# Performance work log

Measured on AMD Instinct MI355X. Metric: run time of the kernel, lower is better.

Reference implementation:

```python
import jax, jax.numpy as jnp
import numpy as np

L, T, R = 2, 2, 2          # layers, node types (0=user,1=movie), edge types
NU, NM, E = 50000, 10000, 500000
C, H, DPHI = 128, 4, 64
D = C // H                 # head dim = 32
SQRT_D = float(np.sqrt(D))


def setup_inputs() -> dict:
    key = jax.random.key(0)
    ks = jax.random.split(key, 16)
    s = 0.05
    src = jax.random.randint(ks[0], (E,), 0, NU)
    dst = jax.random.randint(ks[1], (E,), 0, NM)
    return {
        "user_emb": jax.random.normal(ks[2], (NU, C)) * 0.01,
        "movie_emb": jax.random.normal(ks[3], (NM, C)) * 0.01,
        "phi": jax.random.normal(ks[4], (NM, DPHI)),
        "meta_w": jax.random.normal(ks[5], (DPHI, C)) * s,
        "meta_b": jnp.zeros((C,)),
        "kw": jax.random.normal(ks[6], (L, T, C, C)) * s,
        "kb": jnp.zeros((L, T, C)),
        "qw": jax.random.normal(ks[7], (L, T, C, C)) * s,
        "qb": jnp.zeros((L, T, C)),
        "vw": jax.random.normal(ks[8], (L, T, C, C)) * s,
        "vb": jnp.zeros((L, T, C)),
        "a_rel": jax.random.normal(ks[9], (L, R, H, D, D)) * s,
        "m_rel": jax.random.normal(ks[10], (L, R, H, D, D)) * s,
        "p_rel": jnp.ones((L, R, H)),
        "ow": jax.random.normal(ks[11], (L, T, C, C)) * s,
        "ob": jnp.zeros((L, T, C)),
        "skip": jnp.ones((L, T)),
        "edge_index": jnp.stack([src, dst]),  # [2,E], row0=user idx, row1=movie idx
    }


def _segment_softmax(logits, seg, n):
    # logits: [E,H], seg: [E] destination node ids
    m = jax.ops.segment_max(logits, seg, num_segments=n)
    e = jnp.exp(logits - m[seg])
    s = jax.ops.segment_sum(e, seg, num_segments=n)
    return e / (s[seg] + 1e-16)


def _hgt_layer(xs, kw, kb, qw, qb, vw, vb, a_rel, m_rel, p_rel, ow, ob, skip, edge_index):
    ns = [x.shape[0] for x in xs]
    k = [(xs[t] @ kw[t] + kb[t]).reshape(ns[t], H, D) for t in range(T)]
    q = [(xs[t] @ qw[t] + qb[t]).reshape(ns[t], H, D) for t in range(T)]
    v = [(xs[t] @ vw[t] + vb[t]).reshape(ns[t], H, D) for t in range(T)]
    # edge types: r=0 user->movie, r=1 movie->user (reverse)
    etypes = [(0, 1, edge_index[0], edge_index[1]),
              (1, 0, edge_index[1], edge_index[0])]
    agg = [jnp.zeros((ns[t], C), dtype=xs[t].dtype) for t in range(T)]
    for r, (st, dt, src, dst) in enumerate(etypes):
        ke = jnp.einsum('nhd,hde->nhe', k[st], a_rel[r])   # per-edge-type key transform
        ve = jnp.einsum('nhd,hde->nhe', v[st], m_rel[r])
        logits = (q[dt][dst] * ke[src]).sum(-1) * p_rel[r] / SQRT_D   # [E,H]
        alpha = _segment_softmax(logits, dst, ns[dt])                  # [E,H]
        msg = (alpha[:, :, None] * ve[src]).reshape(-1, C)
        agg[dt] = agg[dt] + jax.ops.segment_sum(msg, dst, num_segments=ns[dt])
    out = []
    for t in range(T):
        o = jax.nn.gelu(agg[t]) @ ow[t] + ob[t]
        g = jax.nn.sigmoid(skip[t])
        out.append(g * o + (1.0 - g) * xs[t])
    return out


def reference(user_emb, movie_emb, phi, meta_w, meta_b, kw, kb, qw, qb, vw, vb,
              a_rel, m_rel, p_rel, ow, ob, skip, edge_index):
    xu = user_emb
    xm = movie_emb + phi @ meta_w + meta_b   # meta feature fusion on movie nodes
    xs = [xu, xm]
    for l in range(L):
        xs = _hgt_layer(xs, kw[l], kb[l], qw[l], qb[l], vw[l], vb[l],
                        a_rel[l], m_rel[l], p_rel[l], ow[l], ob[l], skip[l], edge_index)
    return (xs[0], xs[1])
```

## Files before the change

kernel.cpp:

```cpp
#include <hip/hip_runtime.h>
#include <hip/hip_bf16.h>

#define Cc 128
#define Hh 4
#define Dd 32
#define DPHI2 64
#define Ll 2
#define Tt 2
#define Rr 2

typedef __hip_bfloat16 bf16;
using short8 = __attribute__((ext_vector_type(8))) short;
using f32x4 = __attribute__((ext_vector_type(4))) float;
using f32x2 = __attribute__((ext_vector_type(2))) float;
typedef _Float16 h2 __attribute__((ext_vector_type(2)));
typedef __fp16 fp16x2 __attribute__((ext_vector_type(2)));

__device__ __forceinline__ unsigned short f2bf(float f) {
  union { float f; unsigned u; } v; v.f = f;
  unsigned r = v.u + 0x7fff + ((v.u >> 16) & 1);
  return (unsigned short)(r >> 16);
}
__device__ __forceinline__ h2 u2h(unsigned u) {
  union { unsigned u; h2 h; } v; v.u = u; return v.h;
}
__device__ __forceinline__ unsigned pkh(float a, float b) {
  union { unsigned u; fp16x2 h; } v;
  v.h = __builtin_amdgcn_cvt_pkrtz(a, b);
  return v.u;
}

__device__ __forceinline__ float fp8_decode1(unsigned char b) {
  unsigned u = b & 0x7f;
  float nrm = __builtin_bit_cast(float, (u << 20) + 0x3C000000u);
  float sub = (float)u * 0.001953125f;
  float v = (u >= 8) ? nrm : sub;
  return (b & 0x80) ? -v : v;
}
template <bool HI>
__device__ __forceinline__ f32x2 fp8x2f(unsigned w) {
#if __has_builtin(__builtin_amdgcn_cvt_pk_f32_fp8)
  return __builtin_amdgcn_cvt_pk_f32_fp8(w, HI);
#else
  unsigned b = HI ? (w >> 16) : (w & 0xffff);
  f32x2 r;
  r[0] = fp8_decode1((unsigned char)b);
  r[1] = fp8_decode1((unsigned char)(b >> 8));
  return r;
#endif
}
#if !__has_builtin(__builtin_amdgcn_cvt_pk_fp8_f32)
__device__ __forceinline__ unsigned char fp8_encode1(float f) {
  unsigned s = (__builtin_bit_cast(unsigned, f) >> 31) << 7;
  float a = fabsf(f);
  a = fminf(a, 448.f);
  unsigned char out;
  if (a < 0.0009765625f) {
    out = 0;
  } else if (a < 0.015625f) {
    out = (unsigned char)(a * 512.f + 0.5f);
  } else {
    unsigned bits = __builtin_bit_cast(unsigned, a);
    int e = (int)(bits >> 23) - 127;
    unsigned m = (bits >> 20) & 7;
    m += (bits >> 19) & 1;
    unsigned ee = (unsigned)(e + 7);
    if (m == 8) { m = 0; ee += 1; }
    if (ee > 15) { ee = 15; m = 6; }
    out = (unsigned char)((ee << 3) | m);
  }
  return out | (unsigned char)s;
}
#endif
__device__ __forceinline__ unsigned pk_fp8x4(float v0, float v1, float v2, float v3) {
#if __has_builtin(__builtin_amdgcn_cvt_pk_fp8_f32)
  int p = __builtin_amdgcn_cvt_pk_fp8_f32(v0, v1, 0, false);
  p = __builtin_amdgcn_cvt_pk_fp8_f32(v2, v3, p, true);
  return (unsigned)p;
#else
  return (unsigned)fp8_encode1(v0) | ((unsigned)fp8_encode1(v1) << 8) |
         ((unsigned)fp8_encode1(v2) << 16) | ((unsigned)fp8_encode1(v3) << 24);
#endif
}

__device__ __forceinline__ float dpp_add_xor1(float x) {
  int v = __builtin_amdgcn_update_dpp(0, __builtin_bit_cast(int, x), 0xB1, 0xF, 0xF, true);
  return x + __builtin_bit_cast(float, v);
}
__device__ __forceinline__ float dpp_add_xor2(float x) {
  int v = __builtin_amdgcn_update_dpp(0, __builtin_bit_cast(int, x), 0x4E, 0xF, 0xF, true);
  return x + __builtin_bit_cast(float, v);
}

__device__ __forceinline__ float gelu_tanh(float x) {
  float u = 0.7978845608028654f * (x + 0.044715f * x * x * x);
  float t = 1.f - 2.f / (__expf(2.f * u) + 1.f);
  return 0.5f * x * (1.f + t);
}

__device__ __forceinline__ void gload_lds16(const void* gsrc, void* lds) {
  __builtin_amdgcn_global_load_lds(
      (const __attribute__((address_space(1))) unsigned int*)gsrc,
      (__attribute__((address_space(3))) unsigned int*)lds, 16, 0, 0);
}

__global__ __launch_bounds__(256) void setup_kernel(
    const int* __restrict__ esrc, const int* __restrict__ edst, int E_, int NM_, int NU_,
    int* __restrict__ cnt, int* __restrict__ eoffm, int* __restrict__ eoffu,
    const float* __restrict__ kw, const float* __restrict__ kb,
    const float* __restrict__ qw, const float* __restrict__ qb,
    const float* __restrict__ vw, const float* __restrict__ vb,
    const float* __restrict__ a_rel, const float* __restrict__ m_rel,
    const float* __restrict__ p_rel, const float* __restrict__ ow,
    const float* __restrict__ ob,
    unsigned short* __restrict__ WT, float* __restrict__ bQKV,
    unsigned short* __restrict__ OWT, float* __restrict__ bO,
    const float* __restrict__ ue, const float* __restrict__ me,
    const float* __restrict__ phi, const float* __restrict__ mw,
    const float* __restrict__ mb,
    float* __restrict__ xout, unsigned short* __restrict__ Xb,
    int HB, int PB) {
  int b = blockIdx.x;
  if (b < HB) {
    int base_e = b * 2048;
#pragma unroll
    for (int j = 0; j < 8; ++j) {
      int e = base_e + j * 256 + (int)threadIdx.x;
      if (e < E_) {
        eoffm[e] = atomicAdd(&cnt[edst[e]], 1);
        eoffu[e] = atomicAdd(&cnt[NM_ + esrc[e]], 1);
      }
    }
    return;
  }
  if (b < HB + PB) {
    int idx = (b - HB) * 2 + (threadIdx.x >> 7);
    int g = idx >> 2, lt = idx & 3;
    int l = lt >> 1, t = lt & 1, r = t;
    int k = threadIdx.x & 127;
    const float inv_sqrt_d = 0.17677669529663687f;
    const float QSCALE = 1.4426950408889634f / 256.f;
    float val, bval;
    if (g < 128) {
      val = qw[((size_t)lt * Cc + k) * Cc + g] * QSCALE;
      bval = qb[(size_t)lt * Cc + g] * QSCALE;
    } else if (g < 384) {
      int isV = (g >= 256);
      int n = g - (isV ? 256 : 128);
      int h = n >> 5, e = n & 31;
      const float* W = (isV ? vw : kw) + (size_t)lt * Cc * Cc;
      const float* bb = (isV ? vb : kb) + (size_t)lt * Cc;
      const float* Ah = (isV ? m_rel : a_rel) + (((size_t)l * Rr + r) * Hh + h) * Dd * Dd;
      float s = 0.f, sb = 0.f;
      for (int d = 0; d < Dd; ++d) {
        float ae = Ah[d * Dd + e];
        s += W[(size_t)k * Cc + h * Dd + d] * ae;
        sb += bb[h * Dd + d] * ae;
      }
      float scale = isV ? 256.f : p_rel[((size_t)l * Rr + r) * Hh + h] * inv_sqrt_d * 256.f;
      val = s * scale;
      bval = sb * scale;
    } else {
      int n = g - 384;
      val = ow[((size_t)lt * Cc + k) * Cc + n];
      bval = ob[(size_t)lt * Cc + n];
    }
    if (g < 384) {
      WT[((size_t)lt * 384 + g) * Cc + k] = f2bf(val);
      if (k == 0) bQKV[(size_t)lt * 384 + g] = bval;
    } else {
      OWT[((size_t)lt * Cc + (g - 384)) * Cc + k] = f2bf(val);
      if (k == 0) bO[(size_t)lt * Cc + (g - 384)] = bval;
    }
    return;
  }
  int i4 = (b - HB - PB) * 256 + threadIdx.x;
  int totalU4 = NU_ * 32;
  float4 s;
  size_t o;
  if (i4 < totalU4) {
    o = (size_t)i4 * 4;
    s = *(const float4*)&ue[o];
  } else {
    int mg = i4 - totalU4;
    if (mg >= NM_ * 32) return;
    int m = mg >> 5, c = (mg & 31) * 4;
    o = (size_t)(NU_ * 32 + mg) * 4;
    s = *(const float4*)&me[(size_t)m * Cc + c];
    float4 bmv = *(const float4*)&mb[c];
    s.x += bmv.x; s.y += bmv.y; s.z += bmv.z; s.w += bmv.w;
    const float* ph = phi + (size_t)m * DPHI2;
#pragma unroll 4
    for (int d = 0; d < DPHI2; ++d) {
      float p = ph[d];
      float4 w4 = *(const float4*)&mw[d * Cc + c];
      s.x += p * w4.x; s.y += p * w4.y; s.z += p * w4.z; s.w += p * w4.w;
    }
  }
  *(float4*)&xout[o] = s;
  uint2 pk;
  pk.x = (unsigned)f2bf(s.x) | ((unsigned)f2bf(s.y) << 16);
  pk.y = (unsigned)f2bf(s.z) | ((unsigned)f2bf(s.w) << 16);
  *(uint2*)&Xb[o] = pk;
}

__global__ __launch_bounds__(256) void scan_p1(const int* __restrict__ cnt, int n,
                                               int* __restrict__ psum) {
  int i0 = blockIdx.x * 1024 + threadIdx.x * 4;
  int s = 0;
#pragma unroll
  for (int j = 0; j < 4; ++j) {
    int i = i0 + j;
    if (i < n) s += cnt[i];
  }
#pragma unroll
  for (int off = 1; off < 64; off <<= 1) s += __shfl_xor(s, off, 64);
  __shared__ int wsum[4];
  if ((threadIdx.x & 63) == 0) wsum[threadIdx.x >> 6] = s;
  __syncthreads();
  if (threadIdx.x == 0) psum[blockIdx.x] = wsum[0] + wsum[1] + wsum[2] + wsum[3];
}
__global__ void scan_p2(int* psum, int nb) {
  if (threadIdx.x == 0 && blockIdx.x == 0) {
    int run = 0;
    for (int i = 0; i < nb; ++i) { int v = psum[i]; psum[i] = run; run += v; }
  }
}
__global__ __launch_bounds__(256) void scan_p3(const int* __restrict__ cnt, int n,
                                               const int* __restrict__ psum,
                                               int* __restrict__ rowptr) {
  __shared__ int sdata[256];
  int i0 = blockIdx.x * 1024 + threadIdx.x * 4;
  int a0 = (i0 + 0 < n) ? cnt[i0 + 0] : 0;
  int a1 = (i0 + 1 < n) ? cnt[i0 + 1] : 0;
  int a2 = (i0 + 2 < n) ? cnt[i0 + 2] : 0;
  int a3 = (i0 + 3 < n) ? cnt[i0 + 3] : 0;
  int s = a0 + a1 + a2 + a3;
  sdata[threadIdx.x] = s;
  __syncthreads();
  for (int off = 1; off < 256; off <<= 1) {
    int t = ((int)threadIdx.x >= off) ? sdata[threadIdx.x - off] : 0;
    __syncthreads();
    sdata[threadIdx.x] += t;
    __syncthreads();
  }
  int run = psum[blockIdx.x] + sdata[threadIdx.x] - s;
  if (i0 + 0 < n) rowptr[i0 + 1] = run + a0;
  if (i0 + 1 < n) rowptr[i0 + 2] = run + a0 + a1;
  if (i0 + 2 < n) rowptr[i0 + 3] = run + a0 + a1 + a2;
  if (i0 + 3 < n) rowptr[i0 + 4] = run + s;
  if (blockIdx.x == 0 && threadIdx.x == 0) rowptr[0] = 0;
}

template <int NCH, int MODE>
__global__ __launch_bounds__(256, 2) void mfma_gemm(
    int NBU_, int NU_, int NM_,
    const bf16* __restrict__ Abase,
    const bf16* __restrict__ WTl, const float* __restrict__ biasl,
    char* __restrict__ Qc, char* __restrict__ KVc,
    float* __restrict__ xout, unsigned short* __restrict__ Xb,
    const float* __restrict__ skipl,
    int GB, const int* __restrict__ esrc, const int* __restrict__ edst, int E_,
    const int* __restrict__ rowptr, const int* __restrict__ eoffm,
    const int* __restrict__ eoffu, int* __restrict__ srcAll) {
  __shared__ char Bs[2][16384];
  if ((int)blockIdx.x >= GB) {
    int e = ((int)blockIdx.x - GB) * 256 + threadIdx.x;
    if (e < E_) {
      int s = esrc[e], d = edst[e];
      srcAll[rowptr[d] + eoffm[e]] = s << 8;
      srcAll[rowptr[NM_ + s] + eoffu[e]] = (NU_ + d) << 8;
    }
    return;
  }
  int bx = blockIdx.x;
  int t, row0, M, base;
  if (bx < NBU_) { t = 0; row0 = bx * 128; M = NU_; base = 0; }
  else { t = 1; row0 = (bx - NBU_) * 128; M = NM_; base = NU_; }
  const char* BT = (const char*)(WTl + (size_t)t * (NCH * 64) * Cc);
  const float* bias = biasl + (size_t)t * (NCH * 64);
  int wid = threadIdx.x >> 6, lane = threadIdx.x & 63;
  int rw = row0 + wid * 32;
  bool wact = rw < M;
  int lr = lane & 15, lk8 = (lane >> 4) * 8;

  auto stage = [&](int ch, int buf) {
    const char* src = BT + (size_t)ch * 16384;
#pragma unroll
    for (int j = 0; j < 4; ++j) {
      int u = wid * 4 + j;
      int d = u * 1024 + lane * 16;
      int g = d ^ (((d >> 8) & 7) << 4);
      gload_lds16(src + g, &Bs[buf][u * 1024]);
    }
  };

  short8 a[2][4];
#pragma unroll
  for (int mt = 0; mt < 2; ++mt) {
    int r = rw + mt * 16 + lr;
    const bf16* ap = Abase + (size_t)(base + r) * Cc + lk8;
#pragma unroll
    for (int kk = 0; kk < 4; ++kk) {
      short8 v = {};
      if (wact && r < M) v = *(const short8*)(ap + kk * 32);
      a[mt][kk] = v;
    }
  }
  float g = 0.f;
  if (MODE == 1) g = 1.f / (1.f + __expf(-skipl[t]));

  stage(0, 0);
#pragma unroll
  for (int ch = 0; ch < NCH; ++ch) {
    int buf = ch & 1;
    __syncthreads();
    if (ch + 1 < NCH) stage(ch + 1, buf ^ 1);
    short8 b[4][4];
#pragma unroll
    for (int nt = 0; nt < 4; ++nt) {
      int r = nt * 16 + lr;
#pragma unroll
      for (int kk = 0; kk < 4; ++kk) {
        int a0 = r * 256 + (lk8 + kk * 32) * 2;
        b[nt][kk] = *(const short8*)(&Bs[buf][a0 ^ ((r & 7) << 4)]);
      }
    }
    f32x4 acc[2][4];
#pragma unroll
    for (int mt = 0; mt < 2; ++mt)
#pragma unroll
      for (int nt = 0; nt < 4; ++nt) acc[mt][nt] = (f32x4){0.f, 0.f, 0.f, 0.f};
#pragma unroll
    for (int kk = 0; kk < 4; ++kk)
#pragma unroll
      for (int mt = 0; mt < 2; ++mt)
#pragma unroll
        for (int nt = 0; nt < 4; ++nt)
          acc[mt][nt] = __builtin_amdgcn_mfma_f32_16x16x32_bf16(
              b[nt][kk], a[mt][kk], acc[mt][nt], 0, 0, 0);
    if (!wact) continue;
#pragma unroll
    for (int mt = 0; mt < 2; ++mt) {
      int r = rw + mt * 16 + lr;
      if (r >= M) continue;
      size_t grow = (size_t)(base + r);
#pragma unroll
      for (int nt = 0; nt < 4; ++nt) {
        int cb = ch * 64 + nt * 16 + 4 * (lane >> 4);
        float4 b4 = *(const float4*)&bias[cb];
        float v0 = acc[mt][nt][0] + b4.x;
        float v1 = acc[mt][nt][1] + b4.y;
        float v2 = acc[mt][nt][2] + b4.z;
        float v3 = acc[mt][nt][3] + b4.w;
        if (MODE == 0) {
          if (cb < Cc) {
            uint2 pk;
            pk.x = pkh(v0, v1); pk.y = pkh(v2, v3);
            *(uint2*)(Qc + grow * 256 + cb * 2) = pk;
          } else {
            int c = cb - 128;
            int isv = c >> 7; c &= 127;
            int off = (c >> 3) * 16 + (c & 7) + isv * 8;
            unsigned pk = pk_fp8x4(v0, v1, v2, v3);
            *(unsigned*)(KVc + grow * 256 + off) = pk;
          }
        } else {
          float* xp = xout + grow * Cc + cb;
          float4 old = *(const float4*)xp;
          float n0 = g * v0 + (1.f - g) * old.x;
          float n1 = g * v1 + (1.f - g) * old.y;
          float n2 = g * v2 + (1.f - g) * old.z;
          float n3 = g * v3 + (1.f - g) * old.w;
          *(float4*)xp = make_float4(n0, n1, n2, n3);
          uint2 pk;
          pk.x = (unsigned)f2bf(n0) | ((unsigned)f2bf(n1) << 16);
          pk.y = (unsigned)f2bf(n2) | ((unsigned)f2bf(n3) << 16);
          *(uint2*)(Xb + grow * Cc + cb) = pk;
        }
      }
    }
  }
}

__global__ __launch_bounds__(256) void agg_kernel(
    const int* __restrict__ rowptr, const int* __restrict__ srcAll,
    const char* __restrict__ Qc, const char* __restrict__ KVc,
    unsigned short* __restrict__ AGGb, int NM_, int NU_) {
  int wid = threadIdx.x >> 6, lane = threadIdx.x & 63;
  int sub = lane & 15, eo = lane >> 4;
  int NT_ = NM_ + NU_;
  int W = (blockIdx.x * 4 + wid) * 4 + eo;
  bool active = W < NT_;
  int Wc = active ? W : NT_ - 1;
  int beg = rowptr[Wc];
  int end = active ? rowptr[Wc + 1] : beg;
  int dnode = (Wc < NM_) ? (NU_ + Wc) : (Wc - NM_);
  int myoff = sub * 16;
  uint4 qv = *(const uint4*)(Qc + (size_t)dnode * 256 + myoff);
  float qf0, qf1, qf2, qf3, qf4, qf5, qf6, qf7;
  {
    h2 t0 = u2h(qv.x), t1 = u2h(qv.y), t2 = u2h(qv.z), t3 = u2h(qv.w);
    qf0 = (float)t0[0]; qf1 = (float)t0[1];
    qf2 = (float)t1[0]; qf3 = (float)t1[1];
    qf4 = (float)t2[0]; qf5 = (float)t2[1];
    qf6 = (float)t3[0]; qf7 = (float)t3[1];
  }
  float acc0 = 0.f, acc1 = 0.f, acc2 = 0.f, acc3 = 0.f;
  float acc4 = 0.f, acc5 = 0.f, acc6 = 0.f, acc7 = 0.f;
  float denom = 0.f;
  const char* KVp = KVc + myoff;

#define CONSUME(KV, WVALID)                                                       \
  {                                                                               \
    f32x2 k01 = fp8x2f<false>((KV).x), k23 = fp8x2f<true>((KV).x);                \
    f32x2 k45 = fp8x2f<false>((KV).y), k67 = fp8x2f<true>((KV).y);                \
    float pA = qf0 * k01[0] + qf1 * k01[1] + qf2 * k23[0] + qf3 * k23[1];         \
    float pB = qf4 * k45[0] + qf5 * k45[1] + qf6 * k67[0] + qf7 * k67[1];         \
    float p = pA + pB;                                                            \
    p = dpp_add_xor1(p);                                                          \
    p = dpp_add_xor2(p);                                                          \
    float w = (WVALID) ? exp2f(p) : 0.f;                                          \
    denom += w;                                                                   \
    f32x2 v01 = fp8x2f<false>((KV).z), v23 = fp8x2f<true>((KV).z);                \
    f32x2 v45 = fp8x2f<false>((KV).w), v67 = fp8x2f<true>((KV).w);                \
    acc0 += w * v01[0]; acc1 += w * v01[1];                                       \
    acc2 += w * v23[0]; acc3 += w * v23[1];                                       \
    acc4 += w * v45[0]; acc5 += w * v45[1];                                       \
    acc6 += w * v67[0]; acc7 += w * v67[1];                                       \
  }

  for (int e = beg; __any(e < end); e += 4) {
    bool v0 = e < end, v1 = (e + 1) < end, v2 = (e + 2) < end, v3 = (e + 3) < end;
    int so0 = srcAll[v0 ? e : 0];
    int so1 = srcAll[v1 ? (e + 1) : 0];
    int so2 = srcAll[v2 ? (e + 2) : 0];
    int so3 = srcAll[v3 ? (e + 3) : 0];
    uint4 kv0 = *(const uint4*)(KVp + (size_t)(unsigned)so0);
    uint4 kv1 = *(const uint4*)(KVp + (size_t)(unsigned)so1);
    uint4 kv2 = *(const uint4*)(KVp + (size_t)(unsigned)so2);
    uint4 kv3 = *(const uint4*)(KVp + (size_t)(unsigned)so3);
    CONSUME(kv0, v0)
    CONSUME(kv1, v1)
    CONSUME(kv2, v2)
    CONSUME(kv3, v3)
  }
#undef CONSUME

  if (active) {
    float inv = 1.f / (denom + 1e-16f) * 0.00390625f;
    float o0 = gelu_tanh(acc0 * inv);
    float o1 = gelu_tanh(acc1 * inv);
    float o2 = gelu_tanh(acc2 * inv);
    float o3 = gelu_tanh(acc3 * inv);
    float o4 = gelu_tanh(acc4 * inv);
    float o5 = gelu_tanh(acc5 * inv);
    float o6 = gelu_tanh(acc6 * inv);
    float o7 = gelu_tanh(acc7 * inv);
    uint4 pk;
    pk.x = (unsigned)f2bf(o0) | ((unsigned)f2bf(o1) << 16);
    pk.y = (unsigned)f2bf(o2) | ((unsigned)f2bf(o3) << 16);
    pk.z = (unsigned)f2bf(o4) | ((unsigned)f2bf(o5) << 16);
    pk.w = (unsigned)f2bf(o6) | ((unsigned)f2bf(o7) << 16);
    *(uint4*)(AGGb + (size_t)dnode * Cc + sub * 8) = pk;
  }
}

extern "C" void kernel_launch(void* const* d_in, const int* in_sizes, int n_in,
                              void* d_out, int out_size, void* d_ws, size_t ws_size,
                              hipStream_t stream) {
  const float* user_emb = (const float*)d_in[0];
  const float* movie_emb = (const float*)d_in[1];
  const float* phi = (const float*)d_in[2];
  const float* meta_w = (const float*)d_in[3];
  const float* meta_b = (const float*)d_in[4];
  const float* kw = (const float*)d_in[5];
  const float* kb = (const float*)d_in[6];
  const float* qw = (const float*)d_in[7];
  const float* qb = (const float*)d_in[8];
  const float* vw = (const float*)d_in[9];
  const float* vb = (const float*)d_in[10];
  const float* a_rel = (const float*)d_in[11];
  const float* m_rel = (const float*)d_in[12];
  const float* p_rel = (const float*)d_in[13];
  const float* ow = (const float*)d_in[14];
  const float* ob = (const float*)d_in[15];
  const float* skip = (const float*)d_in[16];
  const int* eidx = (const int*)d_in[17];

  int NU = in_sizes[0] / Cc;
  int NM = in_sizes[1] / Cc;
  int E_ = in_sizes[17] / 2;
  int NT = NU + NM;
  const int* esrc = eidx;
  const int* edst = eidx + E_;

  char* ws = (char*)d_ws;
  size_t off = 0;
  auto alloc = [&](size_t bytes) -> char* {
    char* p = ws + off;
    off = (off + bytes + 255) & ~(size_t)255;
    return p;
  };
  char* Qc = alloc((size_t)NT * 256);
  char* KVc = alloc((size_t)NT * 256);
  unsigned short* Xb = (unsigned short*)alloc((size_t)NT * Cc * 2);
  unsigned short* AGGb = (unsigned short*)alloc((size_t)NT * Cc * 2);
  unsigned short* WT = (unsigned short*)alloc((size_t)Ll * Tt * 384 * Cc * 2);
  unsigned short* OWT = (unsigned short*)alloc((size_t)Ll * Tt * Cc * Cc * 2);
  float* bQKV = (float*)alloc((size_t)Ll * Tt * 384 * 4);
  float* bO = (float*)alloc((size_t)Ll * Tt * Cc * 4);
  int* rowptr = (int*)alloc((size_t)(NT + 1) * 4);
  int* srcAll = (int*)alloc((size_t)2 * E_ * 4);
  int* eoffm = (int*)alloc((size_t)E_ * 4);
  int* eoffu = (int*)alloc((size_t)E_ * 4);
  int* cnt = (int*)alloc((size_t)NT * 4);
  int* psum = (int*)alloc((size_t)256 * 4);
  float* xout = (float*)d_out;

  int nblk = (NT + 1023) / 1024;
  int HB = (E_ + 2047) / 2048;
  int PB = 1024;
  int IB = (NT * 32 + 255) / 256;

  hipMemsetAsync(cnt, 0, (size_t)NT * 4, stream);
  setup_kernel<<<HB + PB + IB, 256, 0, stream>>>(
      esrc, edst, E_, NM, NU, cnt, eoffm, eoffu,
      kw, kb, qw, qb, vw, vb, a_rel, m_rel, p_rel, ow, ob,
      WT, bQKV, OWT, bO,
      user_emb, movie_emb, phi, meta_w, meta_b, xout, Xb, HB, PB);
  scan_p1<<<nblk, 256, 0, stream>>>(cnt, NT, psum);
  scan_p2<<<1, 64, 0, stream>>>(psum, nblk);
  scan_p3<<<nblk, 256, 0, stream>>>(cnt, NT, psum, rowptr);

  int NBU = (NU + 127) / 128;
  int NBM = (NM + 127) / 128;
  int GB = NBU + NBM;
  int nagg = (NT + 15) / 16;
  for (int l = 0; l < Ll; ++l) {
    int extra = (l == 0) ? (E_ + 255) / 256 : 0;
    mfma_gemm<6, 0><<<GB + extra, 256, 0, stream>>>(
        NBU, NU, NM, (const bf16*)Xb, (const bf16*)(WT + (size_t)l * 2 * 384 * Cc),
        bQKV + (size_t)l * 2 * 384, Qc, KVc, nullptr, nullptr, nullptr,
        GB, esrc, edst, (l == 0) ? E_ : 0, rowptr, eoffm, eoffu, srcAll);
    agg_kernel<<<nagg, 256, 0, stream>>>(rowptr, srcAll, Qc, KVc, AGGb, NM, NU);
    mfma_gemm<2, 1><<<GB, 256, 0, stream>>>(
        NBU, NU, NM, (const bf16*)AGGb, (const bf16*)(OWT + (size_t)l * 2 * Cc * Cc),
        bO + (size_t)l * 2 * Cc, nullptr, nullptr, xout, Xb, skip + (size_t)l * 2,
        GB, nullptr, nullptr, 0, nullptr, nullptr, nullptr, nullptr);
  }
}
```

Baseline: 263.5 us.

## Replace global atomic histogram with range-partitioned LDS atomic counting

Edge degree counting and per-edge slot assignment now run in blocks that each own a range of 512 destination nodes. Each block scans the whole edge array and applies shared-memory atomics only for edges that fall in its range, then writes its counts to global memory, which removes the memset and the contended global atomics. The cost is that every block reads all E indices (about 118 blocks each reading 2MB), so global read traffic rises sharply.

```diff
diff --git a/kernel.cpp b/kernel.cpp
--- a/kernel.cpp
+++ b/kernel.cpp
@@ -8,6 +8,7 @@
 #define Ll 2
 #define Tt 2
 #define Rr 2
+#define RNG 512
 
 typedef __hip_bfloat16 bf16;
 using short8 = __attribute__((ext_vector_type(8))) short;
@@ -119,22 +120,42 @@
     const float* __restrict__ phi, const float* __restrict__ mw,
     const float* __restrict__ mb,
     float* __restrict__ xout, unsigned short* __restrict__ Xb,
-    int HB, int PB) {
+    int HBm, int HBT, int PB) {
+  __shared__ int cl[RNG];
   int b = blockIdx.x;
-  if (b < HB) {
-    int base_e = b * 2048;
-#pragma unroll
-    for (int j = 0; j < 8; ++j) {
-      int e = base_e + j * 256 + (int)threadIdx.x;
-      if (e < E_) {
-        eoffm[e] = atomicAdd(&cnt[edst[e]], 1);
-        eoffu[e] = atomicAdd(&cnt[NM_ + esrc[e]], 1);
+  if (b < HBT) {
+    int isU = (b >= HBm);
+    int r0 = (isU ? (b - HBm) : b) * RNG;
+    const int* arr = isU ? esrc : edst;
+    int* eoff = isU ? eoffu : eoffm;
+    int rmax = isU ? NU_ : NM_;
+    int cb = isU ? NM_ : 0;
+    for (int i = threadIdx.x; i < RNG; i += 256) cl[i] = 0;
+    __syncthreads();
+    for (int e0 = (int)threadIdx.x * 4; e0 < E_; e0 += 1024) {
+      if (e0 + 4 <= E_) {
+        int4 v = *(const int4*)(arr + e0);
+        int a0 = v.x - r0, a1 = v.y - r0, a2 = v.z - r0, a3 = v.w - r0;
+        if ((unsigned)a0 < RNG) eoff[e0 + 0] = atomicAdd(&cl[a0], 1);
+        if ((unsigned)a1 < RNG) eoff[e0 + 1] = atomicAdd(&cl[a1], 1);
+        if ((unsigned)a2 < RNG) eoff[e0 + 2] = atomicAdd(&cl[a2], 1);
+        if ((unsigned)a3 < RNG) eoff[e0 + 3] = atomicAdd(&cl[a3], 1);
+      } else {
+        for (int e = e0; e < E_; ++e) {
+          int a = arr[e] - r0;
+          if ((unsigned)a < RNG) eoff[e] = atomicAdd(&cl[a], 1);
+        }
       }
     }
+    __syncthreads();
+    for (int i = threadIdx.x; i < RNG; i += 256) {
+      int r = r0 + i;
+      if (r < rmax) cnt[cb + r] = cl[i];
+    }
     return;
   }
-  if (b < HB + PB) {
-    int idx = (b - HB) * 2 + (threadIdx.x >> 7);
+  if (b < HBT + PB) {
+    int idx = (b - HBT) * 2 + (threadIdx.x >> 7);
     int g = idx >> 2, lt = idx & 3;
     int l = lt >> 1, t = lt & 1, r = t;
     int k = threadIdx.x & 127;
@@ -174,7 +195,7 @@
     }
     return;
   }
-  int i4 = (b - HB - PB) * 256 + threadIdx.x;
+  int i4 = (b - HBT - PB) * 256 + threadIdx.x;
   int totalU4 = NU_ * 32;
   float4 s;
   size_t o;
@@ -519,16 +540,17 @@
   float* xout = (float*)d_out;
 
   int nblk = (NT + 1023) / 1024;
-  int HB = (E_ + 2047) / 2048;
+  int HBm = (NM + RNG - 1) / RNG;
+  int HBu = (NU + RNG - 1) / RNG;
+  int HBT = HBm + HBu;
   int PB = 1024;
   int IB = (NT * 32 + 255) / 256;
 
-  hipMemsetAsync(cnt, 0, (size_t)NT * 4, stream);
-  setup_kernel<<<HB + PB + IB, 256, 0, stream>>>(
+  setup_kernel<<<HBT + PB + IB, 256, 0, stream>>>(
       esrc, edst, E_, NM, NU, cnt, eoffm, eoffu,
       kw, kb, qw, qb, vw, vb, a_rel, m_rel, p_rel, ow, ob,
       WT, bQKV, OWT, bO,
-      user_emb, movie_emb, phi, meta_w, meta_b, xout, Xb, HB, PB);
+      user_emb, movie_emb, phi, meta_w, meta_b, xout, Xb, HBm, HBT, PB);
   scan_p1<<<nblk, 256, 0, stream>>>(cnt, NT, psum);
   scan_p2<<<1, 64, 0, stream>>>(psum, nblk);
   scan_p3<<<nblk, 256, 0, stream>>>(cnt, NT, psum, rowptr);
```

Measured after the change: 487.6 us. 85.0% more time.

## Overlap edge histogram atomics with layer-0 QKV GEMM, move scatter to own kernel

Applied to the files above, without the earlier changes.

Moves the per-edge atomic degree counting out of the setup kernel and into extra blocks of the first QKV GEMM launch, so the histogram runs alongside the GEMM. The CSR scan now runs after that GEMM, and the edge scatter into srcAll gets its own kernel launched before the first aggregation. The aim is to shorten the setup critical path by overlapping the atomic-heavy edge pass with matrix work. In exchange it adds one kernel launch, and the atomics may compete with the GEMM for memory bandwidth.

```diff
diff --git a/kernel.cpp b/kernel.cpp
--- a/kernel.cpp
+++ b/kernel.cpp
@@ -104,9 +104,8 @@
       (__attribute__((address_space(3))) unsigned int*)lds, 16, 0, 0);
 }
 
-__global__ __launch_bounds__(256) void setup_kernel(
-    const int* __restrict__ esrc, const int* __restrict__ edst, int E_, int NM_, int NU_,
-    int* __restrict__ cnt, int* __restrict__ eoffm, int* __restrict__ eoffu,
+__global__ __launch_bounds__(256) void prep_init_kernel(
+    int NM_, int NU_,
     const float* __restrict__ kw, const float* __restrict__ kb,
     const float* __restrict__ qw, const float* __restrict__ qb,
     const float* __restrict__ vw, const float* __restrict__ vb,
@@ -119,22 +118,10 @@
     const float* __restrict__ phi, const float* __restrict__ mw,
     const float* __restrict__ mb,
     float* __restrict__ xout, unsigned short* __restrict__ Xb,
-    int HB, int PB) {
+    int PB) {
   int b = blockIdx.x;
-  if (b < HB) {
-    int base_e = b * 2048;
-#pragma unroll
-    for (int j = 0; j < 8; ++j) {
-      int e = base_e + j * 256 + (int)threadIdx.x;
-      if (e < E_) {
-        eoffm[e] = atomicAdd(&cnt[edst[e]], 1);
-        eoffu[e] = atomicAdd(&cnt[NM_ + esrc[e]], 1);
-      }
-    }
-    return;
-  }
-  if (b < HB + PB) {
-    int idx = (b - HB) * 2 + (threadIdx.x >> 7);
+  if (b < PB) {
+    int idx = b * 2 + (threadIdx.x >> 7);
     int g = idx >> 2, lt = idx & 3;
     int l = lt >> 1, t = lt & 1, r = t;
     int k = threadIdx.x & 127;
@@ -174,7 +161,7 @@
     }
     return;
   }
-  int i4 = (b - HB - PB) * 256 + threadIdx.x;
+  int i4 = (b - PB) * 256 + threadIdx.x;
   int totalU4 = NU_ * 32;
   float4 s;
   size_t o;
@@ -252,6 +239,18 @@
   if (blockIdx.x == 0 && threadIdx.x == 0) rowptr[0] = 0;
 }
 
+__global__ void scatter_kernel(const int* __restrict__ esrc, const int* __restrict__ edst,
+                               int E_, const int* __restrict__ rowptr,
+                               const int* __restrict__ eoffm, const int* __restrict__ eoffu,
+                               int* __restrict__ srcAll, int NU_, int NM_) {
+  int e = blockIdx.x * 256 + threadIdx.x;
+  if (e < E_) {
+    int s = esrc[e], d = edst[e];
+    srcAll[rowptr[d] + eoffm[e]] = s << 8;
+    srcAll[rowptr[NM_ + s] + eoffu[e]] = (NU_ + d) << 8;
+  }
+}
+
 template <int NCH, int MODE>
 __global__ __launch_bounds__(256, 2) void mfma_gemm(
     int NBU_, int NU_, int NM_,
@@ -261,15 +260,17 @@
     float* __restrict__ xout, unsigned short* __restrict__ Xb,
     const float* __restrict__ skipl,
     int GB, const int* __restrict__ esrc, const int* __restrict__ edst, int E_,
-    const int* __restrict__ rowptr, const int* __restrict__ eoffm,
-    const int* __restrict__ eoffu, int* __restrict__ srcAll) {
+    int* __restrict__ cnt, int* __restrict__ eoffm, int* __restrict__ eoffu) {
   __shared__ char Bs[2][16384];
   if ((int)blockIdx.x >= GB) {
-    int e = ((int)blockIdx.x - GB) * 256 + threadIdx.x;
-    if (e < E_) {
-      int s = esrc[e], d = edst[e];
-      srcAll[rowptr[d] + eoffm[e]] = s << 8;
-      srcAll[rowptr[NM_ + s] + eoffu[e]] = (NU_ + d) << 8;
+    int base_e = ((int)blockIdx.x - GB) * 2048;
+#pragma unroll
+    for (int j = 0; j < 8; ++j) {
+      int e = base_e + j * 256 + (int)threadIdx.x;
+      if (e < E_) {
+        eoffm[e] = atomicAdd(&cnt[edst[e]], 1);
+        eoffu[e] = atomicAdd(&cnt[NM_ + esrc[e]], 1);
+      }
     }
     return;
   }
@@ -519,34 +520,41 @@
   float* xout = (float*)d_out;
 
   int nblk = (NT + 1023) / 1024;
-  int HB = (E_ + 2047) / 2048;
   int PB = 1024;
   int IB = (NT * 32 + 255) / 256;
-
-  hipMemsetAsync(cnt, 0, (size_t)NT * 4, stream);
-  setup_kernel<<<HB + PB + IB, 256, 0, stream>>>(
-      esrc, edst, E_, NM, NU, cnt, eoffm, eoffu,
-      kw, kb, qw, qb, vw, vb, a_rel, m_rel, p_rel, ow, ob,
-      WT, bQKV, OWT, bO,
-      user_emb, movie_emb, phi, meta_w, meta_b, xout, Xb, HB, PB);
-  scan_p1<<<nblk, 256, 0, stream>>>(cnt, NT, psum);
-  scan_p2<<<1, 64, 0, stream>>>(psum, nblk);
-  scan_p3<<<nblk, 256, 0, stream>>>(cnt, NT, psum, rowptr);
+  int HB = (E_ + 2047) / 2048;
 
   int NBU = (NU + 127) / 128;
   int NBM = (NM + 127) / 128;
   int GB = NBU + NBM;
   int nagg = (NT + 15) / 16;
-  for (int l = 0; l < Ll; ++l) {
-    int extra = (l == 0) ? (E_ + 255) / 256 : 0;
-    mfma_gemm<6, 0><<<GB + extra, 256, 0, stream>>>(
-        NBU, NU, NM, (const bf16*)Xb, (const bf16*)(WT + (size_t)l * 2 * 384 * Cc),
-        bQKV + (size_t)l * 2 * 384, Qc, KVc, nullptr, nullptr, nullptr,
-        GB, esrc, edst, (l == 0) ? E_ : 0, rowptr, eoffm, eoffu, srcAll);
-    agg_kernel<<<nagg, 256, 0, stream>>>(rowptr, srcAll, Qc, KVc, AGGb, NM, NU);
-    mfma_gemm<2, 1><<<GB, 256, 0, stream>>>(
-        NBU, NU, NM, (const bf16*)AGGb, (const bf16*)(OWT + (size_t)l * 2 * Cc * Cc),
-        bO + (size_t)l * 2 * Cc, nullptr, nullptr, xout, Xb, skip + (size_t)l * 2,
-        GB, nullptr, nullptr, 0, nullptr, nullptr, nullptr, nullptr);
-  }
-}
+  int SB = (E_ + 255) / 256;
+
+  hipMemsetAsync(cnt, 0, (size_t)NT * 4, stream);
+  prep_init_kernel<<<PB + IB, 256, 0, stream>>>(
+      NM, NU, kw, kb, qw, qb, vw, vb, a_rel, m_rel, p_rel, ow, ob,
+      WT, bQKV, OWT, bO,
+      user_emb, movie_emb, phi, meta_w, meta_b, xout, Xb, PB);
+  mfma_gemm<6, 0><<<GB + HB, 256, 0, stream>>>(
+      NBU, NU, NM, (const bf16*)Xb, (const bf16*)WT, bQKV, Qc, KVc,
+      nullptr, nullptr, nullptr, GB, esrc, edst, E_, cnt, eoffm, eoffu);
+  scan_p1<<<nblk, 256, 0, stream>>>(cnt, NT, psum);
+  scan_p2<<<1, 64, 0, stream>>>(psum, nblk);
+  scan_p3<<<nblk, 256, 0, stream>>>(cnt, NT, psum, rowptr);
+  scatter_kernel<<<SB, 256, 0, stream>>>(esrc, edst, E_, rowptr, eoffm, eoffu,
+                                         srcAll, NU, NM);
+  agg_kernel<<<nagg, 256, 0, stream>>>(rowptr, srcAll, Qc, KVc, AGGb, NM, NU);
+  mfma_gemm<2, 1><<<GB, 256, 0, stream>>>(
+      NBU, NU, NM, (const bf16*)AGGb, (const bf16*)OWT, bO,
+      nullptr, nullptr, xout, Xb, skip, GB, nullptr, nullptr, 0,
+      nullptr, nullptr, nullptr);
+  mfma_gemm<6, 0><<<GB, 256, 0, stream>>>(
+      NBU, NU, NM, (const bf16*)Xb, (const bf16*)(WT + (size_t)2 * 384 * Cc),
+      bQKV + (size_t)2 * 384, Qc, KVc, nullptr, nullptr, nullptr,
+      GB, nullptr, nullptr, 0, nullptr, nullptr, nullptr);
+  agg_kernel<<<nagg, 256, 0, stream>>>(rowptr, srcAll, Qc, KVc, AGGb, NM, NU);
+  mfma_gemm<2, 1><<<GB, 256, 0, stream>>>(
+      NBU, NU, NM, (const bf16*)AGGb, (const bf16*)(OWT + (size_t)2 * Cc * Cc),
+      bO + (size_t)2 * Cc, nullptr, nullptr, xout, Xb, skip + 2,
+      GB, nullptr, nullptr, 0, nullptr, nullptr, nullptr);
+}
```

Result: no change. 265.6 us (+0.8%).
